# Kernel tuning notes

Measured on AMD Instinct MI355X. Metric: run time of the kernel, lower is better.

## Reference

```python
import jax, jax.numpy as jnp
import numpy as np

HID = 32
NUM_GRAPHS = 256
N_NODES = 100000


def graph_conv(x, src, dst, ew, rel_w, rel_b, root_w):
    # PyG GraphConv: out = lin_rel(sum_{j in N(i)} e_ji * x_j) + lin_root(x_i)
    msg = x[src] * ew[:, None]                                  # [E, F] gather
    agg = jax.ops.segment_sum(msg, dst, num_segments=N_NODES)    # [N, F] scatter-add
    return agg @ rel_w + rel_b + x @ root_w


def setup_inputs() -> dict:
    key = jax.random.key(0)
    ks = jax.random.split(key, 16)
    N, E, F = N_NODES, 1600000, 64
    x = jax.random.normal(ks[0], (N, F), dtype=jnp.float32)
    edge_index = jax.random.randint(ks[1], (2, E), 0, N, dtype=jnp.int64)
    edge_attr = jax.random.uniform(ks[2], (E,), dtype=jnp.float32)
    batch = jnp.sort(jax.random.randint(ks[3], (N,), 0, NUM_GRAPHS, dtype=jnp.int64))
    s = lambda k, shp: jax.random.normal(k, shp, dtype=jnp.float32) * 0.1
    return {
        "x": x, "edge_index": edge_index, "edge_attr": edge_attr, "batch": batch,
        "conv1_rel_w": s(ks[4], (F, HID)), "conv1_rel_b": jnp.zeros((HID,), jnp.float32),
        "conv1_root_w": s(ks[5], (F, HID)),
        "conv2_rel_w": s(ks[6], (HID, HID)), "conv2_rel_b": jnp.zeros((HID,), jnp.float32),
        "conv2_root_w": s(ks[7], (HID, HID)),
        "lin1_w": s(ks[8], (HID, 32)), "lin1_b": jnp.zeros((32,), jnp.float32),
        "lin2_w": s(ks[9], (32, 16)), "lin2_b": jnp.zeros((16,), jnp.float32),
        "lin_w": s(ks[10], (16, 1)), "lin_b": jnp.zeros((1,), jnp.float32),
    }


def reference(x, edge_index, edge_attr, batch,
              conv1_rel_w, conv1_rel_b, conv1_root_w,
              conv2_rel_w, conv2_rel_b, conv2_root_w,
              lin1_w, lin1_b, lin2_w, lin2_b, lin_w, lin_b):
    src, dst = edge_index[0], edge_index[1]
    h = jax.nn.relu(graph_conv(x, src, dst, edge_attr, conv1_rel_w, conv1_rel_b, conv1_root_w))
    h = jax.nn.relu(graph_conv(h, src, dst, edge_attr, conv2_rel_w, conv2_rel_b, conv2_root_w))
    # global mean pool over graphs
    sums = jax.ops.segment_sum(h, batch, num_segments=NUM_GRAPHS)          # [G, 32]
    cnts = jax.ops.segment_sum(jnp.ones((h.shape[0],), h.dtype), batch, num_segments=NUM_GRAPHS)
    g = sums / jnp.maximum(cnts, 1.0)[:, None]
    # dropout is identity in eval mode
    g = jax.nn.relu(g @ lin1_w + lin1_b)
    g = g @ lin2_w + lin2_b
    g = jax.nn.relu(g)
    return g @ lin_w + lin_b  # [G, 1]
```

## Files before the change

### kernel.cpp

```cpp
#include <hip/hip_runtime.h>
#include <hip/hip_fp16.h>

#define NGRAPH 256
#define FIN 64
#define HID 32
#define NB_SHIFT 8
#define NB_NODES 256
#define KMAX2 512
#define EPB 2048
#define EPT 8
#define NT 64
#define XPAD 65
#define HPAD 33
#define PCAP 6016

union SU {
    int h[KMAX2];
    struct { float Wr[FIN * HID]; float Wo[FIN * HID]; float b[HID];
             float x[NT * XPAD]; } g;
};

__global__ __launch_bounds__(256, 4) void hist_lin64(
    const int* __restrict__ dst, int* __restrict__ cbb, int E, int K, int NBLK,
    const float* __restrict__ x, const float* __restrict__ Wrel,
    const float* __restrict__ Wroot, const float* __restrict__ bias,
    __half* __restrict__ A, float* __restrict__ B, int N)
{
    __shared__ SU u;
    int tid = threadIdx.x;
    if (blockIdx.x < (unsigned)NBLK) {
        for (int i = tid; i < K; i += 256) u.h[i] = 0;
        __syncthreads();
        int e0 = blockIdx.x * EPB + tid * 8;
        if (e0 + 7 < E) {
            int4 d0 = *reinterpret_cast<const int4*>(dst + e0);
            int4 d1 = *reinterpret_cast<const int4*>(dst + e0 + 4);
            atomicAdd(&u.h[d0.x >> NB_SHIFT], 1); atomicAdd(&u.h[d0.y >> NB_SHIFT], 1);
            atomicAdd(&u.h[d0.z >> NB_SHIFT], 1); atomicAdd(&u.h[d0.w >> NB_SHIFT], 1);
            atomicAdd(&u.h[d1.x >> NB_SHIFT], 1); atomicAdd(&u.h[d1.y >> NB_SHIFT], 1);
            atomicAdd(&u.h[d1.z >> NB_SHIFT], 1); atomicAdd(&u.h[d1.w >> NB_SHIFT], 1);
        } else {
            for (int e = e0; e < E && e < e0 + 8; ++e)
                atomicAdd(&u.h[dst[e] >> NB_SHIFT], 1);
        }
        __syncthreads();
        for (int i = tid; i < K; i += 256)
            cbb[(size_t)i * NBLK + blockIdx.x] = u.h[i];
        return;
    }
    {
        const float4* Wr4 = (const float4*)Wrel;
        const float4* Wo4 = (const float4*)Wroot;
        for (int i = tid; i < FIN * HID / 4; i += 256) {
            ((float4*)u.g.Wr)[i] = Wr4[i];
            ((float4*)u.g.Wo)[i] = Wo4[i];
        }
        if (tid < HID) u.g.b[tid] = bias[tid];
    }
    int base = (blockIdx.x - NBLK) * NT;
    {
        const float4* x4 = (const float4*)x;
        for (int i = tid; i < NT * 16; i += 256) {
            int row = i >> 4, c4 = i & 15;
            int n = base + row;
            float4 v = (n < N) ? x4[(size_t)n * 16 + c4]
                               : make_float4(0.f, 0.f, 0.f, 0.f);
            *(float4*)&u.g.x[row * XPAD + c4 * 4] = v;
        }
    }
    __syncthreads();

    int nl = tid >> 3;
    int fq = (tid & 7) * 4;
    const float* xa = &u.g.x[nl * XPAD];
    const float* xb = &u.g.x[(nl + 32) * XPAD];
    float4 ar0 = make_float4(0.f,0.f,0.f,0.f), ao0 = ar0;
    float4 ar1 = ar0, ao1 = ar0;
    #pragma unroll 4
    for (int k = 0; k < FIN; ++k) {
        float4 w4 = *(const float4*)&u.g.Wr[k * HID + fq];
        float4 o4 = *(const float4*)&u.g.Wo[k * HID + fq];
        float va = xa[k], vb = xb[k];
        ar0.x = fmaf(va, w4.x, ar0.x); ar0.y = fmaf(va, w4.y, ar0.y);
        ar0.z = fmaf(va, w4.z, ar0.z); ar0.w = fmaf(va, w4.w, ar0.w);
        ao0.x = fmaf(va, o4.x, ao0.x); ao0.y = fmaf(va, o4.y, ao0.y);
        ao0.z = fmaf(va, o4.z, ao0.z); ao0.w = fmaf(va, o4.w, ao0.w);
        ar1.x = fmaf(vb, w4.x, ar1.x); ar1.y = fmaf(vb, w4.y, ar1.y);
        ar1.z = fmaf(vb, w4.z, ar1.z); ar1.w = fmaf(vb, w4.w, ar1.w);
        ao1.x = fmaf(vb, o4.x, ao1.x); ao1.y = fmaf(vb, o4.y, ao1.y);
        ao1.z = fmaf(vb, o4.z, ao1.z); ao1.w = fmaf(vb, o4.w, ao1.w);
    }
    float4 bb = *(const float4*)&u.g.b[fq];
    int n0 = base + nl, n1 = base + nl + 32;
    if (n0 < N) {
        __half2 pa = __floats2half2_rn(ar0.x, ar0.y);
        __half2 pb = __floats2half2_rn(ar0.z, ar0.w);
        uint2 pk; pk.x = *(unsigned*)&pa; pk.y = *(unsigned*)&pb;
        *(uint2*)&A[(size_t)n0 * HID + fq] = pk;
        ao0.x += bb.x; ao0.y += bb.y; ao0.z += bb.z; ao0.w += bb.w;
        *(float4*)&B[(size_t)n0 * HID + fq] = ao0;
    }
    if (n1 < N) {
        __half2 pa = __floats2half2_rn(ar1.x, ar1.y);
        __half2 pb = __floats2half2_rn(ar1.z, ar1.w);
        uint2 pk; pk.x = *(unsigned*)&pa; pk.y = *(unsigned*)&pb;
        *(uint2*)&A[(size_t)n1 * HID + fq] = pk;
        ao1.x += bb.x; ao1.y += bb.y; ao1.z += bb.z; ao1.w += bb.w;
        *(float4*)&B[(size_t)n1 * HID + fq] = ao1;
    }
}

__global__ __launch_bounds__(256, 4) void node_lin32(
    const float* __restrict__ Hpre, const float* __restrict__ Wrel,
    const float* __restrict__ Wroot, const float* __restrict__ bias,
    __half* __restrict__ A, float* __restrict__ C, int N)
{
    __shared__ float sWr[HID * HID];
    __shared__ float sWo[HID * HID];
    __shared__ float sb[HID];
    __shared__ float sh[NT * HPAD];
    int tid = threadIdx.x;
    {
        const float4* Wr4 = (const float4*)Wrel;
        const float4* Wo4 = (const float4*)Wroot;
        for (int i = tid; i < HID * HID / 4; i += 256) {
            ((float4*)sWr)[i] = Wr4[i];
            ((float4*)sWo)[i] = Wo4[i];
        }
        if (tid < HID) sb[tid] = bias[tid];
    }
    int base = blockIdx.x * NT;
    {
        const float4* H4 = (const float4*)Hpre;
        for (int i = tid; i < NT * 8; i += 256) {
            int row = i >> 3, c4 = i & 7;
            int n = base + row;
            float4 v = make_float4(0.f, 0.f, 0.f, 0.f);
            if (n < N) {
                v = H4[(size_t)n * 8 + c4];
                v.x = v.x > 0.f ? v.x : 0.f; v.y = v.y > 0.f ? v.y : 0.f;
                v.z = v.z > 0.f ? v.z : 0.f; v.w = v.w > 0.f ? v.w : 0.f;
            }
            *(float4*)&sh[row * HPAD + c4 * 4] = v;
        }
    }
    __syncthreads();

    int nl = tid >> 3;
    int fq = (tid & 7) * 4;
    const float* xa = &sh[nl * HPAD];
    const float* xb = &sh[(nl + 32) * HPAD];
    float4 ar0 = make_float4(0.f,0.f,0.f,0.f), ao0 = ar0;
    float4 ar1 = ar0, ao1 = ar0;
    #pragma unroll 4
    for (int k = 0; k < HID; ++k) {
        float4 w4 = *(const float4*)&sWr[k * HID + fq];
        float4 o4 = *(const float4*)&sWo[k * HID + fq];
        float va = xa[k], vb = xb[k];
        ar0.x = fmaf(va, w4.x, ar0.x); ar0.y = fmaf(va, w4.y, ar0.y);
        ar0.z = fmaf(va, w4.z, ar0.z); ar0.w = fmaf(va, w4.w, ar0.w);
        ao0.x = fmaf(va, o4.x, ao0.x); ao0.y = fmaf(va, o4.y, ao0.y);
        ao0.z = fmaf(va, o4.z, ao0.z); ao0.w = fmaf(va, o4.w, ao0.w);
        ar1.x = fmaf(vb, w4.x, ar1.x); ar1.y = fmaf(vb, w4.y, ar1.y);
        ar1.z = fmaf(vb, w4.z, ar1.z); ar1.w = fmaf(vb, w4.w, ar1.w);
        ao1.x = fmaf(vb, o4.x, ao1.x); ao1.y = fmaf(vb, o4.y, ao1.y);
        ao1.z = fmaf(vb, o4.z, ao1.z); ao1.w = fmaf(vb, o4.w, ao1.w);
    }
    float4 bb = *(const float4*)&sb[fq];
    int n0 = base + nl, n1 = base + nl + 32;
    if (n0 < N) {
        __half2 pa = __floats2half2_rn(ar0.x, ar0.y);
        __half2 pb = __floats2half2_rn(ar0.z, ar0.w);
        uint2 pk; pk.x = *(unsigned*)&pa; pk.y = *(unsigned*)&pb;
        *(uint2*)&A[(size_t)n0 * HID + fq] = pk;
        ao0.x += bb.x; ao0.y += bb.y; ao0.z += bb.z; ao0.w += bb.w;
        *(float4*)&C[(size_t)n0 * HID + fq] = ao0;
    }
    if (n1 < N) {
        __half2 pa = __floats2half2_rn(ar1.x, ar1.y);
        __half2 pb = __floats2half2_rn(ar1.z, ar1.w);
        uint2 pk; pk.x = *(unsigned*)&pa; pk.y = *(unsigned*)&pb;
        *(uint2*)&A[(size_t)n1 * HID + fq] = pk;
        ao1.x += bb.x; ao1.y += bb.y; ao1.z += bb.z; ao1.w += bb.w;
        *(float4*)&C[(size_t)n1 * HID + fq] = ao1;
    }
}


__global__ __launch_bounds__(256) void bucket_scan(
    int* __restrict__ cbb, int* __restrict__ btot, int NBLK)
{
    __shared__ int sc[256];
    size_t row = (size_t)blockIdx.x * NBLK;
    int t = threadIdx.x;
    int base = t * 4;
    int v[4]; int s = 0;
    #pragma unroll
    for (int j = 0; j < 4; ++j) { v[j] = (base + j < NBLK) ? cbb[row + base + j] : 0; s += v[j]; }
    sc[t] = s;
    __syncthreads();
    int acc = s;
    for (int off = 1; off < 256; off <<= 1) {
        int add = (t >= off) ? sc[t - off] : 0;
        __syncthreads();
        acc += add;
        sc[t] = acc;
        __syncthreads();
    }
    int run = acc - s;
    #pragma unroll
    for (int j = 0; j < 4; ++j) {
        if (base + j < NBLK) cbb[row + base + j] = run;
        run += v[j];
    }
    if (t == 255) btot[blockIdx.x] = acc;
}

__global__ __launch_bounds__(256) void btot_scan(
    const int* __restrict__ btot, int* __restrict__ bbase, int K)
{
    __shared__ int sc[256];
    int t = threadIdx.x;
    int base = t * 4;
    int v[4]; int s = 0;
    #pragma unroll
    for (int j = 0; j < 4; ++j) { v[j] = (base + j < K) ? btot[base + j] : 0; s += v[j]; }
    sc[t] = s;
    __syncthreads();
    int acc = s;
    for (int off = 1; off < 256; off <<= 1) {
        int add = (t >= off) ? sc[t - off] : 0;
        __syncthreads();
        acc += add;
        sc[t] = acc;
        __syncthreads();
    }
    int run = acc - s;
    #pragma unroll
    for (int j = 0; j < 4; ++j) {
        if (base + j < K) bbase[base + j] = run;
        run += v[j];
    }
    if (t == 255) bbase[K] = acc;
}

__global__ __launch_bounds__(256) void partB(
    const int* __restrict__ src, const int* __restrict__ dst,
    const float* __restrict__ ew, const int* __restrict__ cbb,
    const int* __restrict__ bbase, int2* __restrict__ stg8,
    int E, int K, int NBLK)
{
    __shared__ int4 pay[EPB];
    __shared__ int h[KMAX2];
    __shared__ int lofs[KMAX2];
    __shared__ int gb[KMAX2];
    __shared__ int sc[256];
    int tid = threadIdx.x;
    for (int i = tid; i < K; i += 256) h[i] = 0;
    __syncthreads();

    int base = blockIdx.x * EPB;
    int es[EPT], ds[EPT]; float wsr[EPT];
    #pragma unroll
    for (int k = 0; k < EPT; ++k) {
        int e = base + k * 256 + tid;
        if (e < E) {
            es[k] = src[e]; ds[k] = dst[e]; wsr[k] = ew[e];
            atomicAdd(&h[ds[k] >> NB_SHIFT], 1);
        } else ds[k] = -1;
    }
    __syncthreads();

    int b0 = tid * 2;
    int v0 = (b0 < K) ? h[b0] : 0;
    int v1 = (b0 + 1 < K) ? h[b0 + 1] : 0;
    int s = v0 + v1;
    sc[tid] = s;
    __syncthreads();
    int acc = s;
    for (int off = 1; off < 256; off <<= 1) {
        int add = (tid >= off) ? sc[tid - off] : 0;
        __syncthreads();
        acc += add;
        sc[tid] = acc;
        __syncthreads();
    }
    int run = acc - s;
    if (b0 < K) lofs[b0] = run;
    if (b0 + 1 < K) lofs[b0 + 1] = run + v0;
    __syncthreads();

    for (int b = tid; b < K; b += 256) {
        gb[b] = bbase[b] + cbb[(size_t)b * NBLK + blockIdx.x];
        h[b] = lofs[b];
    }
    __syncthreads();

    #pragma unroll
    for (int k = 0; k < EPT; ++k) {
        if (ds[k] >= 0) {
            int b = ds[k] >> NB_SHIFT;
            int dloc = ds[k] & (NB_NODES - 1);
            int slot = atomicAdd(&h[b], 1);
            pay[slot] = make_int4(es[k] | (dloc << 17), __float_as_int(wsr[k]),
                                  gb[b] + slot - lofs[b], 0);
        }
    }
    __syncthreads();

    int tot = E - base; if (tot > EPB) tot = EPB;
    for (int i = tid; i < tot; i += 256) {
        int4 p = pay[i];
        stg8[p.z] = make_int2(p.x, p.y);
    }
}

__global__ __launch_bounds__(512) void partC2(
    const int2* __restrict__ stg8, const int* __restrict__ bbase,
    int* __restrict__ rowptr, int2* __restrict__ perm, int N, int K)
{
    __shared__ int2 pe[PCAP];
    __shared__ int hcnt[NB_NODES];
    __shared__ int hinc[NB_NODES];
    int b = blockIdx.x;
    int n0 = b << NB_SHIFT;
    int nTop = n0 + NB_NODES; if (nTop > N) nTop = N;
    int nloc = nTop - n0;
    int tid = threadIdx.x;
    if (tid < NB_NODES) hcnt[tid] = 0;
    int lo = bbase[b], hi = bbase[b + 1];
    int sz = hi - lo;
    bool fit = (sz <= PCAP);
    if (fit) {
        for (int i = tid; i < sz; i += 512) pe[i] = stg8[lo + i];
    }
    __syncthreads();
    if (fit) {
        for (int i = tid; i < sz; i += 512)
            atomicAdd(&hcnt[pe[i].x >> 17], 1);
    } else {
        for (int e = lo + tid; e < hi; e += 512)
            atomicAdd(&hcnt[stg8[e].x >> 17], 1);
    }
    __syncthreads();
    if (tid < NB_NODES) hinc[tid] = hcnt[tid];
    __syncthreads();
    for (int off = 1; off < NB_NODES; off <<= 1) {
        int v = (tid < NB_NODES && tid >= off) ? hinc[tid - off] : 0;
        __syncthreads();
        if (tid < NB_NODES) hinc[tid] += v;
        __syncthreads();
    }
    if (tid < nloc) {
        int excl = hinc[tid] - hcnt[tid];
        rowptr[n0 + tid] = lo + excl;
        hcnt[tid] = excl;
    }
    if (b == K - 1 && tid == 0) rowptr[N] = hi;
    __syncthreads();
    if (fit) {
        for (int i = tid; i < sz; i += 512) {
            int2 p = pe[i];
            int pos = lo + atomicAdd(&hcnt[p.x >> 17], 1);
            perm[pos] = make_int2(p.x & 0x1FFFF, p.y);
        }
    } else {
        for (int e = lo + tid; e < hi; e += 512) {
            int2 p = stg8[e];
            int pos = lo + atomicAdd(&hcnt[p.x >> 17], 1);
            perm[pos] = make_int2(p.x & 0x1FFFF, p.y);
        }
    }
}

__global__ __launch_bounds__(256) void csr_agg(
    const int* __restrict__ rowptr, const int2* __restrict__ perm,
    const __half* __restrict__ A, float* __restrict__ out, int N)
{
    int gid = blockIdx.x * 256 + threadIdx.x;
    int n = gid >> 2;
    if (n >= N) return;
    int q = threadIdx.x & 3;
    int e0 = rowptr[n], e1 = rowptr[n + 1];
    const uint4* A4 = (const uint4*)A;
    float a0[8] = {0.f,0.f,0.f,0.f,0.f,0.f,0.f,0.f};
    float a1[8] = {0.f,0.f,0.f,0.f,0.f,0.f,0.f,0.f};
    int e = e0;
    for (; e + 1 < e1; e += 2) {
        int2 p0 = perm[e];
        int2 p1 = perm[e + 1];
        uint4 r0 = A4[(size_t)p0.x * 4 + q];
        uint4 r1 = A4[(size_t)p1.x * 4 + q];
        float w0 = __int_as_float(p0.y), w1 = __int_as_float(p1.y);
        float2 c0 = __half22float2(*(__half2*)&r0.x);
        float2 c1 = __half22float2(*(__half2*)&r0.y);
        float2 c2 = __half22float2(*(__half2*)&r0.z);
        float2 c3 = __half22float2(*(__half2*)&r0.w);
        a0[0] = fmaf(c0.x, w0, a0[0]); a0[1] = fmaf(c0.y, w0, a0[1]);
        a0[2] = fmaf(c1.x, w0, a0[2]); a0[3] = fmaf(c1.y, w0, a0[3]);
        a0[4] = fmaf(c2.x, w0, a0[4]); a0[5] = fmaf(c2.y, w0, a0[5]);
        a0[6] = fmaf(c3.x, w0, a0[6]); a0[7] = fmaf(c3.y, w0, a0[7]);
        float2 d0 = __half22float2(*(__half2*)&r1.x);
        float2 d1 = __half22float2(*(__half2*)&r1.y);
        float2 d2 = __half22float2(*(__half2*)&r1.z);
        float2 d3 = __half22float2(*(__half2*)&r1.w);
        a1[0] = fmaf(d0.x, w1, a1[0]); a1[1] = fmaf(d0.y, w1, a1[1]);
        a1[2] = fmaf(d1.x, w1, a1[2]); a1[3] = fmaf(d1.y, w1, a1[3]);
        a1[4] = fmaf(d2.x, w1, a1[4]); a1[5] = fmaf(d2.y, w1, a1[5]);
        a1[6] = fmaf(d3.x, w1, a1[6]); a1[7] = fmaf(d3.y, w1, a1[7]);
    }
    if (e < e1) {
        int2 p = perm[e];
        uint4 r = A4[(size_t)p.x * 4 + q];
        float w = __int_as_float(p.y);
        float2 c0 = __half22float2(*(__half2*)&r.x);
        float2 c1 = __half22float2(*(__half2*)&r.y);
        float2 c2 = __half22float2(*(__half2*)&r.z);
        float2 c3 = __half22float2(*(__half2*)&r.w);
        a0[0] = fmaf(c0.x, w, a0[0]); a0[1] = fmaf(c0.y, w, a0[1]);
        a0[2] = fmaf(c1.x, w, a0[2]); a0[3] = fmaf(c1.y, w, a0[3]);
        a0[4] = fmaf(c2.x, w, a0[4]); a0[5] = fmaf(c2.y, w, a0[5]);
        a0[6] = fmaf(c3.x, w, a0[6]); a0[7] = fmaf(c3.y, w, a0[7]);
    }
    #pragma unroll
    for (int i = 0; i < 8; ++i) a0[i] += a1[i];
    float4* O4 = (float4*)out;
    size_t oi = (size_t)n * 8 + q * 2;
    float4 o = O4[oi];
    o.x += a0[0]; o.y += a0[1]; o.z += a0[2]; o.w += a0[3];
    O4[oi] = o;
    float4 p = O4[oi + 1];
    p.x += a0[4]; p.y += a0[5]; p.z += a0[6]; p.w += a0[7];
    O4[oi + 1] = p;
}

__global__ __launch_bounds__(256) void pool_mlp(
    const float* __restrict__ C, const int* __restrict__ batch, int N,
    const float* __restrict__ W1, const float* __restrict__ b1,
    const float* __restrict__ W2, const float* __restrict__ b2,
    const float* __restrict__ W3, const float* __restrict__ b3,
    float* __restrict__ out)
{
    int g = blockIdx.x;
    int tid = threadIdx.x;
    int lo, hi;
    {
        int l = 0, r = N;
        while (l < r) { int m = (l + r) >> 1; if (batch[m] < g) l = m + 1; else r = m; }
        lo = l;
        r = N;
        while (l < r) { int m = (l + r) >> 1; if (batch[m] < g + 1) l = m + 1; else r = m; }
        hi = l;
    }
    __shared__ float ssum[8][32];
    __shared__ float gvec[32];
    __shared__ float h1v[32];
    __shared__ float h2v[16];
    int f = tid & 31, seg = tid >> 5;
    float acc = 0.f;
    for (int n = lo + seg; n < hi; n += 8) {
        float v = C[(size_t)n * HID + f];
        acc += v > 0.f ? v : 0.f;
    }
    ssum[seg][f] = acc;
    __syncthreads();
    if (tid < 32) {
        float s = 0.f;
        #pragma unroll
        for (int k = 0; k < 8; ++k) s += ssum[k][tid];
        float c = (float)(hi - lo); c = c > 1.f ? c : 1.f;
        gvec[tid] = s / c;
    }
    __syncthreads();
    if (tid < 32) {
        float a = b1[tid];
        #pragma unroll
        for (int k = 0; k < 32; ++k) a = fmaf(gvec[k], W1[k * 32 + tid], a);
        h1v[tid] = a > 0.f ? a : 0.f;
    }
    __syncthreads();
    if (tid < 16) {
        float a = b2[tid];
        #pragma unroll
        for (int k = 0; k < 32; ++k) a = fmaf(h1v[k], W2[k * 16 + tid], a);
        h2v[tid] = a > 0.f ? a : 0.f;
    }
    __syncthreads();
    if (tid == 0) {
        float o = b3[0];
        #pragma unroll
        for (int k = 0; k < 16; ++k) o = fmaf(h2v[k], W3[k], o);
        out[g] = o;
    }
}

extern "C" void kernel_launch(void* const* d_in, const int* in_sizes, int n_in,
                              void* d_out, int out_size, void* d_ws, size_t ws_size,
                              hipStream_t stream) {
    const float* x     = (const float*)d_in[0];
    const int*   ei    = (const int*)d_in[1];
    const float* ew    = (const float*)d_in[2];
    const int*   batch = (const int*)d_in[3];
    const float* c1rw  = (const float*)d_in[4];
    const float* c1rb  = (const float*)d_in[5];
    const float* c1ow  = (const float*)d_in[6];
    const float* c2rw  = (const float*)d_in[7];
    const float* c2rb  = (const float*)d_in[8];
    const float* c2ow  = (const float*)d_in[9];
    const float* l1w   = (const float*)d_in[10];
    const float* l1b   = (const float*)d_in[11];
    const float* l2w   = (const float*)d_in[12];
    const float* l2b   = (const float*)d_in[13];
    const float* lw    = (const float*)d_in[14];
    const float* lb    = (const float*)d_in[15];

    int N = in_sizes[0] / FIN;
    int E = in_sizes[2];
    const int* src = ei;
    const int* dst = ei + E;
    int K    = (N + NB_NODES - 1) >> NB_SHIFT;
    int NBLK = (E + EPB - 1) / EPB;

    char* ws = (char*)d_ws;
    size_t off = 0;
    auto alloc = [&](size_t nbytes) { void* p = ws + off; off += (nbytes + 255) & ~size_t(255); return p; };
    __half* A      = (__half*)alloc((size_t)N * HID * 2);
    float*  BC     = (float*) alloc((size_t)N * HID * 4);
    int2*   perm   = (int2*)  alloc((size_t)E * 8);
    int2*   stg8   = (int2*)  alloc((size_t)E * 8);
    int*    cbb    = (int*)   alloc((size_t)K * NBLK * 4);
    int*    rowptr = (int*)   alloc((size_t)(N + 1) * 4);
    int*    btot   = (int*)   alloc((size_t)KMAX2 * 4);
    int*    bbase  = (int*)   alloc((size_t)(KMAX2 + 1) * 4);

    int nb_node = (N + NT - 1) / NT;
    int nb_agg  = (int)(((long long)N * 4 + 255) / 256);

    hist_lin64<<<NBLK + nb_node, 256, 0, stream>>>(
        dst, cbb, E, K, NBLK, x, c1rw, c1ow, c1rb, A, BC, N);
    bucket_scan<<<K, 256, 0, stream>>>(cbb, btot, NBLK);
    btot_scan<<<1, 256, 0, stream>>>(btot, bbase, K);
    partB<<<NBLK, 256, 0, stream>>>(src, dst, ew, cbb, bbase, stg8, E, K, NBLK);
    partC2<<<K, 512, 0, stream>>>(stg8, bbase, rowptr, perm, N, K);

    csr_agg<<<nb_agg, 256, 0, stream>>>(rowptr, perm, A, BC, N);
    node_lin32<<<nb_node, 256, 0, stream>>>(BC, c2rw, c2ow, c2rb, A, BC, N);
    csr_agg<<<nb_agg, 256, 0, stream>>>(rowptr, perm, A, BC, N);
    pool_mlp<<<NGRAPH, 256, 0, stream>>>(BC, batch, N, l1w, l1b, l2w, l2b, lw, lb,
                                         (float*)d_out);
}
```

Baseline: 159.1 us.

## Double edges per block in bucket partition and shrink shared staging payload

```diff
diff --git a/kernel.cpp b/kernel.cpp
--- a/kernel.cpp
+++ b/kernel.cpp
@@ -7,8 +7,7 @@
 #define NB_SHIFT 8
 #define NB_NODES 256
 #define KMAX2 512
-#define EPB 2048
-#define EPT 8
+#define EPB 4096
 #define NT 64
 #define XPAD 65
 #define HPAD 33
@@ -31,16 +30,18 @@
     if (blockIdx.x < (unsigned)NBLK) {
         for (int i = tid; i < K; i += 256) u.h[i] = 0;
         __syncthreads();
-        int e0 = blockIdx.x * EPB + tid * 8;
-        if (e0 + 7 < E) {
-            int4 d0 = *reinterpret_cast<const int4*>(dst + e0);
-            int4 d1 = *reinterpret_cast<const int4*>(dst + e0 + 4);
-            atomicAdd(&u.h[d0.x >> NB_SHIFT], 1); atomicAdd(&u.h[d0.y >> NB_SHIFT], 1);
-            atomicAdd(&u.h[d0.z >> NB_SHIFT], 1); atomicAdd(&u.h[d0.w >> NB_SHIFT], 1);
-            atomicAdd(&u.h[d1.x >> NB_SHIFT], 1); atomicAdd(&u.h[d1.y >> NB_SHIFT], 1);
-            atomicAdd(&u.h[d1.z >> NB_SHIFT], 1); atomicAdd(&u.h[d1.w >> NB_SHIFT], 1);
+        int e0 = blockIdx.x * EPB + tid * 16;
+        if (e0 + 15 < E) {
+            #pragma unroll
+            for (int c = 0; c < 4; ++c) {
+                int4 d = *reinterpret_cast<const int4*>(dst + e0 + c * 4);
+                atomicAdd(&u.h[d.x >> NB_SHIFT], 1);
+                atomicAdd(&u.h[d.y >> NB_SHIFT], 1);
+                atomicAdd(&u.h[d.z >> NB_SHIFT], 1);
+                atomicAdd(&u.h[d.w >> NB_SHIFT], 1);
+            }
         } else {
-            for (int e = e0; e < E && e < e0 + 8; ++e)
+            for (int e = e0; e < E && e < e0 + 16; ++e)
                 atomicAdd(&u.h[dst[e] >> NB_SHIFT], 1);
         }
         __syncthreads();
@@ -244,26 +245,27 @@
     if (t == 255) bbase[K] = acc;
 }
 
-__global__ __launch_bounds__(256) void partB(
+__global__ __launch_bounds__(512) void partB(
     const int* __restrict__ src, const int* __restrict__ dst,
     const float* __restrict__ ew, const int* __restrict__ cbb,
     const int* __restrict__ bbase, int2* __restrict__ stg8,
     int E, int K, int NBLK)
 {
-    __shared__ int4 pay[EPB];
+    __shared__ int2 pay[EPB];
+    __shared__ unsigned short bid[EPB];
     __shared__ int h[KMAX2];
     __shared__ int lofs[KMAX2];
     __shared__ int gb[KMAX2];
-    __shared__ int sc[256];
+    __shared__ int sc[512];
     int tid = threadIdx.x;
-    for (int i = tid; i < K; i += 256) h[i] = 0;
+    for (int i = tid; i < K; i += 512) h[i] = 0;
     __syncthreads();
 
     int base = blockIdx.x * EPB;
-    int es[EPT], ds[EPT]; float wsr[EPT];
-    #pragma unroll
-    for (int k = 0; k < EPT; ++k) {
-        int e = base + k * 256 + tid;
+    int es[8], ds[8]; float wsr[8];
+    #pragma unroll
+    for (int k = 0; k < 8; ++k) {
+        int e = base + k * 512 + tid;
         if (e < E) {
             es[k] = src[e]; ds[k] = dst[e]; wsr[k] = ew[e];
             atomicAdd(&h[ds[k] >> NB_SHIFT], 1);
@@ -271,47 +273,42 @@
     }
     __syncthreads();
 
-    int b0 = tid * 2;
-    int v0 = (b0 < K) ? h[b0] : 0;
-    int v1 = (b0 + 1 < K) ? h[b0 + 1] : 0;
-    int s = v0 + v1;
-    sc[tid] = s;
-    __syncthreads();
-    int acc = s;
-    for (int off = 1; off < 256; off <<= 1) {
+    int v0 = (tid < K) ? h[tid] : 0;
+    sc[tid] = v0;
+    __syncthreads();
+    int acc = v0;
+    for (int off = 1; off < 512; off <<= 1) {
         int add = (tid >= off) ? sc[tid - off] : 0;
         __syncthreads();
         acc += add;
         sc[tid] = acc;
         __syncthreads();
     }
-    int run = acc - s;
-    if (b0 < K) lofs[b0] = run;
-    if (b0 + 1 < K) lofs[b0 + 1] = run + v0;
-    __syncthreads();
-
-    for (int b = tid; b < K; b += 256) {
+    if (tid < K) lofs[tid] = acc - v0;
+    __syncthreads();
+
+    for (int b = tid; b < K; b += 512) {
         gb[b] = bbase[b] + cbb[(size_t)b * NBLK + blockIdx.x];
         h[b] = lofs[b];
     }
     __syncthreads();
 
     #pragma unroll
-    for (int k = 0; k < EPT; ++k) {
+    for (int k = 0; k < 8; ++k) {
         if (ds[k] >= 0) {
             int b = ds[k] >> NB_SHIFT;
             int dloc = ds[k] & (NB_NODES - 1);
             int slot = atomicAdd(&h[b], 1);
-            pay[slot] = make_int4(es[k] | (dloc << 17), __float_as_int(wsr[k]),
-                                  gb[b] + slot - lofs[b], 0);
+            pay[slot] = make_int2(es[k] | (dloc << 17), __float_as_int(wsr[k]));
+            bid[slot] = (unsigned short)b;
         }
     }
     __syncthreads();
 
     int tot = E - base; if (tot > EPB) tot = EPB;
-    for (int i = tid; i < tot; i += 256) {
-        int4 p = pay[i];
-        stg8[p.z] = make_int2(p.x, p.y);
+    for (int i = tid; i < tot; i += 512) {
+        int b = bid[i];
+        stg8[gb[b] + i - lofs[b]] = pay[i];
     }
 }
 
@@ -540,7 +537,7 @@
         dst, cbb, E, K, NBLK, x, c1rw, c1ow, c1rb, A, BC, N);
     bucket_scan<<<K, 256, 0, stream>>>(cbb, btot, NBLK);
     btot_scan<<<1, 256, 0, stream>>>(btot, bbase, K);
-    partB<<<NBLK, 256, 0, stream>>>(src, dst, ew, cbb, bbase, stg8, E, K, NBLK);
+    partB<<<NBLK, 512, 0, stream>>>(src, dst, ew, cbb, bbase, stg8, E, K, NBLK);
     partC2<<<K, 512, 0, stream>>>(stg8, bbase, rowptr, perm, N, K);
 
     csr_agg<<<nb_agg, 256, 0, stream>>>(rowptr, perm, A, BC, N);
```

Result: faster. 153.7 us (-3.4%).
